# Kernel optimization log

Hardware: AMD Instinct MI355X
Metric: run time of the kernel (lower is better)

Reference implementation:

```python
import jax, jax.numpy as jnp
import numpy as np

B, C_IN, C_HID, H, W = 4, 512, 512, 64, 64


def setup_inputs() -> dict:
    key = jax.random.key(0)
    ks = jax.random.split(key, 9)
    s_in = 1.0 / np.sqrt(C_IN)
    s_hid = 1.0 / np.sqrt(C_HID)
    return {
        "inp": jax.random.normal(ks[0], (B, C_IN, H, W), dtype=jnp.float32),
        "Wk": jax.random.normal(ks[1], (C_HID, C_IN), dtype=jnp.float32) * s_in,
        "bk": jax.random.normal(ks[2], (C_HID,), dtype=jnp.float32) * 0.01,
        "Wq": jax.random.normal(ks[3], (C_HID, C_IN), dtype=jnp.float32) * s_in,
        "bq": jax.random.normal(ks[4], (C_HID,), dtype=jnp.float32) * 0.01,
        "Wv": jax.random.normal(ks[5], (C_HID, C_IN), dtype=jnp.float32) * s_in,
        "bv": jax.random.normal(ks[6], (C_HID,), dtype=jnp.float32) * 0.01,
        "Wo": jax.random.normal(ks[7], (C_IN, C_HID), dtype=jnp.float32) * s_hid,
        "bo": jax.random.normal(ks[8], (C_IN,), dtype=jnp.float32) * 0.01,
    }


def reference(inp, Wk, bk, Wq, bq, Wv, bv, Wo, bo):
    b, _, h, w = inp.shape
    n = h * w

    def conv1x1(x, Wt, bias):  # 1x1 conv == per-pixel GEMM
        return jnp.einsum('bchw,oc->bohw', x, Wt) + bias[None, :, None, None]

    k = conv1x1(inp, Wk, bk).reshape(b, C_HID, n)   # [B,Ch,N]
    q = conv1x1(inp, Wq, bq).reshape(b, C_HID, n)
    v = conv1x1(inp, Wv, bv).reshape(b, C_HID, n)

    scale = 1.0 / jnp.sqrt(jnp.asarray(C_HID, dtype=jnp.float32))
    # weight[b,i,j] = <key_i, query_j> / sqrt(Ch); softmax over j (dim=2)
    scores = jnp.einsum('bci,bcj->bij', k, q) * scale  # [B,N,N]
    weight = jax.nn.softmax(scores, axis=2)
    # out[b,c,i] = sum_j weight[b,i,j] * v[b,c,j]
    out = jnp.einsum('bij,bcj->bci', weight, v).reshape(b, C_HID, h, w)
    return conv1x1(out, Wo, bo)  # [B,C_in,H,W]
```

## Files before the change

### kernel.cpp

```cpp
#include <hip/hip_runtime.h>
#include <hip/hip_bf16.h>


typedef __attribute__((ext_vector_type(4))) float f32x4;
typedef __attribute__((ext_vector_type(8))) short short8;
typedef __attribute__((ext_vector_type(4))) short short4v;

#define QSCALE 0.06376639774f
#define FENCE asm volatile("" ::: "memory")
#define SBAR  __builtin_amdgcn_s_barrier()

__device__ __forceinline__ unsigned short f2bf(float f) {
  unsigned u = __builtin_bit_cast(unsigned, f);
  unsigned r = (u + 0x7FFFu + ((u >> 16) & 1u)) >> 16;
  return (unsigned short)r;
}

__device__ __forceinline__ void gll16(const void* g, void* l) {
  __builtin_amdgcn_global_load_lds((const __attribute__((address_space(1))) void*)g,
                                   (__attribute__((address_space(3))) void*)l, 16, 0, 0);
}

#define MFMA_BF16(d, va, vb) \
  d = __builtin_amdgcn_mfma_f32_16x16x32_bf16(va, vb, d, 0, 0, 0)

__device__ __forceinline__ void gemm256_core(
    const short* __restrict__ A, int lda,
    const short* __restrict__ B, int ldb,
    int nkt, char* sm, f32x4 (&acc)[8][4]) {
  const int tid = threadIdx.x, w = tid >> 6, lane = tid & 63;
  const int g = lane >> 4, l15 = lane & 15;
  const int wm = w >> 2, wn = w & 3;
  const int swz = (l15 & 7) << 4;
  const int brow = (wn & 1) << 6;

  auto stageA = [&](int buf, int h, int kt) {
    char* dst = sm + (((buf << 1) | h) << 14) + (w << 10);
    const char* gs = (const char*)A + ((size_t)(h * 128) * lda + (size_t)kt * 64) * 2;
#pragma unroll
    for (int q = 0; q < 2; ++q) {
      int o = (q << 13) | (w << 10) | (lane << 4);
      int row = o >> 7, cb = (o & 127) ^ ((row & 7) << 4);
      gll16(gs + (size_t)row * (lda * 2) + cb, dst + (q << 13));
    }
  };
  auto stageB = [&](int buf, int h, int kt) {
    char* dst = sm + 65536 + (((buf << 1) | h) << 14) + (w << 10);
    const char* gs = (const char*)B + ((size_t)(h * 128) * ldb + (size_t)kt * 64) * 2;
#pragma unroll
    for (int q = 0; q < 2; ++q) {
      int o = (q << 13) | (w << 10) | (lane << 4);
      int row = o >> 7, cb = (o & 127) ^ ((row & 7) << 4);
      gll16(gs + (size_t)row * (ldb * 2) + cb, dst + (q << 13));
    }
  };

  stageA(0, 0, 0); stageA(0, 1, 0); stageB(0, 0, 0); stageB(0, 1, 0);
  stageA(1, 0, 1); stageA(1, 1, 1); stageB(1, 0, 1); stageB(1, 1, 1);
  asm volatile("s_waitcnt vmcnt(8)" ::: "memory");
  SBAR; FENCE;

  for (int t = 0; t < nkt; ++t) {
    const int buf = t & 1;
    const char* SA = sm + (((buf << 1) | wm) << 14);
    const char* SB = sm + 65536 + (((buf << 1) | (wn >> 1)) << 14);
    short8 a[8][2], b[4][2];
#pragma unroll
    for (int mf = 0; mf < 8; ++mf)
      a[mf][0] = *(const short8*)(SA + (mf * 16 + l15) * 128 + ((g * 16) ^ swz));
#pragma unroll
    for (int nf = 0; nf < 4; ++nf)
      b[nf][0] = *(const short8*)(SB + (brow + nf * 16 + l15) * 128 + ((g * 16) ^ swz));
#pragma unroll
    for (int mf = 0; mf < 8; ++mf)
      a[mf][1] = *(const short8*)(SA + (mf * 16 + l15) * 128 + ((64 + g * 16) ^ swz));
#pragma unroll
    for (int nf = 0; nf < 4; ++nf)
      b[nf][1] = *(const short8*)(SB + (brow + nf * 16 + l15) * 128 + ((64 + g * 16) ^ swz));
    __builtin_amdgcn_s_setprio(1);
#pragma unroll
    for (int mf = 0; mf < 4; ++mf)
#pragma unroll
      for (int nf = 0; nf < 4; ++nf)
        MFMA_BF16(acc[mf][nf], a[mf][0], b[nf][0]);
    __builtin_amdgcn_s_setprio(0);
    asm volatile("s_waitcnt lgkmcnt(0)" ::: "memory");
    SBAR; FENCE;
    if (t + 2 < nkt) { stageA(buf, 0, t + 2); stageA(buf, 1, t + 2); }
    __builtin_amdgcn_s_setprio(1);
#pragma unroll
    for (int mf = 4; mf < 8; ++mf)
#pragma unroll
      for (int nf = 0; nf < 4; ++nf)
        MFMA_BF16(acc[mf][nf], a[mf][0], b[nf][0]);
    __builtin_amdgcn_s_setprio(0);
    if (t + 2 < nkt) { stageB(buf, 0, t + 2); stageB(buf, 1, t + 2); }
    __builtin_amdgcn_s_setprio(1);
#pragma unroll
    for (int mf = 0; mf < 4; ++mf)
#pragma unroll
      for (int nf = 0; nf < 4; ++nf)
        MFMA_BF16(acc[mf][nf], a[mf][1], b[nf][1]);
#pragma unroll
    for (int mf = 4; mf < 8; ++mf)
#pragma unroll
      for (int nf = 0; nf < 4; ++nf)
        MFMA_BF16(acc[mf][nf], a[mf][1], b[nf][1]);
    __builtin_amdgcn_s_setprio(0);
    if (t + 2 < nkt)      asm volatile("s_waitcnt vmcnt(8)" ::: "memory");
    else if (t + 1 < nkt) asm volatile("s_waitcnt vmcnt(0)" ::: "memory");
    SBAR; FENCE;
  }
}

#define BOUNCE256_WRITE(smp, row, colb, val) \
  *(short*)((smp) + (row) * 512 + (((colb)) ^ (((row) & 7) << 4))) = (val)

__device__ __forceinline__ void bounce256_flush(const char* smp, short* gbase,
                                                int pitch ) {
  const int tid = threadIdx.x;
  SBAR; FENCE;
#pragma unroll
  for (int it = 0; it < 16; ++it) {
    int row = (tid >> 5) + it * 16;
    short8 v = *(const short8*)(smp + row * 512 + (((tid & 31) * 16) ^ ((row & 7) << 4)));
    *(short8*)(gbase + (size_t)row * pitch + (tid & 31) * 8) = v;
  }
}

__device__ __forceinline__ void gemm_core(const short* __restrict__ A, int lda,
                                          const short* __restrict__ B, int ldb,
                                          int nk, short* lds, f32x4 (&acc)[4][4]) {
  const int tid = threadIdx.x, w = tid >> 6, lane = tid & 63;
  const int g = lane >> 4, l15 = lane & 15;
  const int wr = w >> 1, wc = w & 1;
  const int rsub = lane >> 2, slot = lane & 3;
  char* la = (char*)lds;
  char* lb = (char*)(lds + 128 * 32);
  for (int ki = 0; ki < nk; ++ki) {
    const int k0 = ki * 32;
    __syncthreads();
#pragma unroll
    for (int q = 0; q < 2; ++q) {
      int qq = w * 2 + q;
      int row = qq * 16 + rsub;
      int soff = ((slot ^ (row & 3)) * 16);
      gll16((const char*)(A + (size_t)row * lda + k0) + soff, la + qq * 1024);
      gll16((const char*)(B + (size_t)row * ldb + k0) + soff, lb + qq * 1024);
    }
    __syncthreads();
    short8 am[4], bn[4];
#pragma unroll
    for (int m = 0; m < 4; ++m) {
      int row = wr * 64 + m * 16 + l15;
      am[m] = *(const short8*)(la + row * 64 + ((g * 16) ^ ((l15 & 3) << 4)));
    }
#pragma unroll
    for (int n = 0; n < 4; ++n) {
      int row = wc * 64 + n * 16 + l15;
      bn[n] = *(const short8*)(lb + row * 64 + ((g * 16) ^ ((l15 & 3) << 4)));
    }
#pragma unroll
    for (int m = 0; m < 4; ++m)
#pragma unroll
      for (int n = 0; n < 4; ++n)
        MFMA_BF16(acc[m][n], am[m], bn[n]);
  }
}

__global__ __launch_bounds__(256) void cvt_w_kernel(
    const float* __restrict__ wk, const float* __restrict__ wq,
    const float* __restrict__ wv, const float* __restrict__ wo,
    short* __restrict__ o) {
  int z = blockIdx.y;
  const float* s = (z == 0) ? wk : (z == 1) ? wq : (z == 2) ? wv : wo;
  int i = blockIdx.x * 256 + threadIdx.x;
  float4 f = ((const float4*)s)[i];
  short4v v;
  v[0] = (short)f2bf(f.x); v[1] = (short)f2bf(f.y);
  v[2] = (short)f2bf(f.z); v[3] = (short)f2bf(f.w);
  if (z < 3) {
    *(short4v*)(o + z * 262144 + i * 4) = v;
  } else {
    int idx = i * 4, co = idx >> 9, cc = idx & 511;
    short* base = o + 786432 + co * 1024 + cc;
    *(short4v*)base = v;
    *(short4v*)(base + 512) = v;
  }
}

__global__ __launch_bounds__(256) void transpose_x_kernel(
    const float* __restrict__ inp, short* __restrict__ xt) {
  __shared__ float t[32][33];
  int tx = threadIdx.x, ty = threadIdx.y;
  int n0 = blockIdx.x * 32, c0 = blockIdx.y * 32, b = blockIdx.z;
  const float* src = inp + ((size_t)(b * 512 + c0)) * 4096 + n0;
#pragma unroll
  for (int r = 0; r < 4; ++r) t[ty + r * 8][tx] = src[(ty + r * 8) * 4096 + tx];
  __syncthreads();
  short* dst = xt + ((size_t)((b << 12) + n0)) * 512 + c0;
#pragma unroll
  for (int r = 0; r < 4; ++r) dst[(ty + r * 8) * 512 + tx] = (short)f2bf(t[tx][ty + r * 8]);
}

__global__ __launch_bounds__(512, 2) void kqv256_kernel(
    const short* __restrict__ xt,
    const short* __restrict__ wk, const short* __restrict__ wq, const short* __restrict__ wv,
    const float* __restrict__ bk, const float* __restrict__ bq, const float* __restrict__ bv,
    short* __restrict__ kt, short* __restrict__ qt, short* __restrict__ vc) {
  extern __shared__ char sm[];
  const int bid = blockIdx.x;
  const int xcd = bid & 7, s = bid >> 3;
  const int pg = s / 6, t = s % 6;
  const int panel = pg * 8 + xcd;
  const int z = (t < 4) ? (t >> 1) : 2;
  const short *A, *B;
  int arow0, brow0;
  if (z < 2) {
    arow0 = panel * 256; brow0 = (t & 1) * 256;
    A = xt + (size_t)arow0 * 512;
    B = ((z == 0) ? wk : wq) + (size_t)brow0 * 512;
  } else {
    arow0 = (t - 4) * 256; brow0 = panel * 256;
    A = wv + (size_t)arow0 * 512;
    B = xt + (size_t)brow0 * 512;
  }
  f32x4 acc[8][4] = {};
  gemm256_core(A, 512, B, 512, 8, sm, acc);
  const int tid = threadIdx.x, w = tid >> 6, lane = tid & 63;
  const int gq = lane >> 4, l15 = lane & 15;
  const int wm = w >> 2, wn = w & 3;
#pragma unroll
  for (int mf = 0; mf < 8; ++mf)
#pragma unroll
    for (int nf = 0; nf < 4; ++nf)
#pragma unroll
      for (int r = 0; r < 4; ++r) {
        int row = wm * 128 + mf * 16 + gq * 4 + r;
        int col = wn * 64 + nf * 16 + l15;
        float v = acc[mf][nf][r], val;
        if (z == 0)      val = (v + bk[brow0 + col]) * QSCALE;
        else if (z == 1) val = v + bq[brow0 + col];
        else             val = v + bv[arow0 + row];
        BOUNCE256_WRITE(sm, row, col * 2, (short)f2bf(val));
      }
  short* gbase; int pitch;
  if (z == 0)      { gbase = kt + (size_t)arow0 * 512 + brow0; pitch = 512; }
  else if (z == 1) { gbase = qt + (size_t)arow0 * 512 + brow0; pitch = 512; }
  else             { gbase = vc + (size_t)arow0 * 16384 + brow0; pitch = 16384; }
  bounce256_flush(sm, gbase, pitch);
}

__global__ __launch_bounds__(512, 2) void gemm_s256_kernel(
    const short* __restrict__ kt, const short* __restrict__ qt,
    short* __restrict__ P, float* __restrict__ Lpart) {
  extern __shared__ char sm[];
  const int bid = blockIdx.x;
  const int xcd = bid & 7, s = bid >> 3;
  const int b = xcd >> 1, h = xcd & 1;
  const int jt0 = (s & 7) * 256, i0 = (s >> 3) * 256;
  const short* A = kt + ((size_t)(b << 12) + i0) * 512;
  const short* B = qt + ((size_t)((b << 12) + h * 2048 + jt0)) * 512;
  f32x4 acc[8][4] = {};
  gemm256_core(A, 512, B, 512, 8, sm, acc);
  const int tid = threadIdx.x, w = tid >> 6, lane = tid & 63;
  const int gq = lane >> 4, l15 = lane & 15;
  const int wm = w >> 2, wn = w & 3;
  const int jp = (h * 2048 + jt0 + wn * 64) >> 6;
  float* Lp = Lpart + (((size_t)b * 64 + jp) << 12) + i0 + wm * 128;
#pragma unroll
  for (int mf = 0; mf < 8; ++mf) {
    float psum[4] = {0.f, 0.f, 0.f, 0.f};
#pragma unroll
    for (int nf = 0; nf < 4; ++nf)
#pragma unroll
      for (int r = 0; r < 4; ++r) {
        float p = exp2f(acc[mf][nf][r]);
        psum[r] += p;
        int row = wm * 128 + mf * 16 + gq * 4 + r;
        int colb = (wn * 64 + nf * 16 + l15) * 2;
        BOUNCE256_WRITE(sm, row, colb, (short)f2bf(p));
      }
#pragma unroll
    for (int r = 0; r < 4; ++r) {
      float ss = psum[r];
      ss += __shfl_xor(ss, 1); ss += __shfl_xor(ss, 2);
      ss += __shfl_xor(ss, 4); ss += __shfl_xor(ss, 8);
      if (l15 == 0) Lp[mf * 16 + gq * 4 + r] = ss;
    }
  }
  short* gbase = P + (size_t)h * 33554432 + ((size_t)((b << 12) + i0)) * 2048 + jt0;
  bounce256_flush(sm, gbase, 2048);
}

__global__ __launch_bounds__(512, 2) void gemm_pv256_kernel(
    const short* __restrict__ P, const short* __restrict__ vc,
    short* __restrict__ otab) {
  extern __shared__ char sm[];
  const int bid = blockIdx.x;
  const int xcd = bid & 7, s = bid >> 3;
  const int b = xcd >> 1, h = xcd & 1;
  const int c0 = (s & 1) * 256, i0 = (s >> 1) * 256;
  const short* A = P + (size_t)h * 33554432 + ((size_t)((b << 12) + i0)) * 2048;
  const short* B = vc + (size_t)c0 * 16384 + (b << 12) + h * 2048;
  f32x4 acc[8][4] = {};
  gemm256_core(A, 2048, B, 16384, 32, sm, acc);
  const int tid = threadIdx.x, w = tid >> 6, lane = tid & 63;
  const int gq = lane >> 4, l15 = lane & 15;
  const int wm = w >> 2, wn = w & 3;
#pragma unroll
  for (int mf = 0; mf < 8; ++mf)
#pragma unroll
    for (int nf = 0; nf < 4; ++nf)
#pragma unroll
      for (int r = 0; r < 4; ++r) {
        int row = wm * 128 + mf * 16 + gq * 4 + r;
        int colb = (wn * 64 + nf * 16 + l15) * 2;
        BOUNCE256_WRITE(sm, row, colb, (short)f2bf(acc[mf][nf][r]));
      }
  short* gbase = otab + ((size_t)((b << 12) + i0)) * 1024 + h * 512 + c0;
  bounce256_flush(sm, gbase, 1024);
}

__global__ __launch_bounds__(256) void lred_kernel(
    const float* __restrict__ Lpart, float* __restrict__ linv) {
  int i = blockIdx.x * 256 + threadIdx.x;
  int b = i >> 12;
  float s = 0.f;
#pragma unroll 8
  for (int jp = 0; jp < 64; ++jp) s += Lpart[(((size_t)b * 64 + jp) << 12) + (i & 4095)];
  linv[i] = 1.0f / s;
}

__global__ __launch_bounds__(256) void gemm_out_kernel(
    const short* __restrict__ wdup, const short* __restrict__ otab,
    const float* __restrict__ bo, const float* __restrict__ linv,
    float* __restrict__ out) {
  __shared__ short lds[2 * 128 * 32];
  const int bid = blockIdx.x;
  const int xcd = bid & 7, s = bid >> 3;
  const int cot = s & 3;
  const int p = (s >> 2) * 8 + xcd;
  const int nt = p & 31, b = p >> 5;
  const int arow0 = cot * 128;
  const int bn0 = nt * 128;
  const short* A = wdup + (size_t)arow0 * 1024;
  const short* B = otab + ((size_t)((b << 12) + bn0)) * 1024;
  f32x4 acc[4][4] = {};
  gemm_core(A, 1024, B, 1024, 32, lds, acc);
  const int tid = threadIdx.x, w = tid >> 6, lane = tid & 63;
  const int g = lane >> 4, l15 = lane & 15;
  const int wr = w >> 1, wc = w & 1;
#pragma unroll
  for (int m = 0; m < 4; ++m) {
    int co = arow0 + wr * 64 + m * 16 + g * 4;
#pragma unroll
    for (int n = 0; n < 4; ++n) {
      int nl = bn0 + wc * 64 + n * 16 + l15;
      float li = linv[(b << 12) + nl];
#pragma unroll
      for (int r = 0; r < 4; ++r)
        out[((size_t)(b * 512 + co + r) << 12) + nl] = acc[m][n][r] * li + bo[co + r];
    }
  }
}

extern "C" void kernel_launch(void* const* d_in, const int* in_sizes, int n_in,
                              void* d_out, int out_size, void* d_ws, size_t ws_size,
                              hipStream_t stream) {
  const float* inp = (const float*)d_in[0];
  const float* Wk = (const float*)d_in[1];
  const float* bk = (const float*)d_in[2];
  const float* Wq = (const float*)d_in[3];
  const float* bq = (const float*)d_in[4];
  const float* Wv = (const float*)d_in[5];
  const float* bv = (const float*)d_in[6];
  const float* Wo = (const float*)d_in[7];
  const float* bo = (const float*)d_in[8];
  float* out = (float*)d_out;
  char* ws = (char*)d_ws;
  const size_t MB = 1048576;
  short* kt    = (short*)(ws);
  short* qt    = (short*)(ws + 16 * MB);
  short* vc    = (short*)(ws + 32 * MB);
  short* wb    = (short*)(ws + 48 * MB);
  short* xt    = (short*)(ws + 51 * MB);
  float* Lpart = (float*)(ws + 51 * MB);
  float* linv  = (float*)(ws + 55 * MB);
  short* P     = (short*)(ws + 67 * MB);
  short* otab  = (short*)(ws + 195 * MB);

  (void)in_sizes; (void)n_in; (void)out_size; (void)ws_size;

  hipFuncSetAttribute((const void*)kqv256_kernel,
                      hipFuncAttributeMaxDynamicSharedMemorySize, 131072);
  hipFuncSetAttribute((const void*)gemm_s256_kernel,
                      hipFuncAttributeMaxDynamicSharedMemorySize, 131072);
  hipFuncSetAttribute((const void*)gemm_pv256_kernel,
                      hipFuncAttributeMaxDynamicSharedMemorySize, 131072);

  cvt_w_kernel<<<dim3(256, 4), 256, 0, stream>>>(Wk, Wq, Wv, Wo, wb);
  transpose_x_kernel<<<dim3(128, 16, 4), dim3(32, 8, 1), 0, stream>>>(inp, xt);
  kqv256_kernel<<<384, 512, 131072, stream>>>(
      xt, wb, wb + 262144, wb + 524288, bk, bq, bv, kt, qt, vc);
  gemm_s256_kernel<<<1024, 512, 131072, stream>>>(kt, qt, P, Lpart);
  gemm_pv256_kernel<<<256, 512, 131072, stream>>>(P, vc, otab);
  lred_kernel<<<64, 256, 0, stream>>>(Lpart, linv);
  gemm_out_kernel<<<512, 256, 0, stream>>>(wb + 786432, otab, bo, linv, out);
}
```

Before: 273.4 us.

## Use fine-grained interleaved staging pipeline in 256 GEMM core and port output GEMM

```diff
diff --git a/kernel.cpp b/kernel.cpp
--- a/kernel.cpp
+++ b/kernel.cpp
@@ -8,7 +8,8 @@
 
 #define QSCALE 0.06376639774f
 #define FENCE asm volatile("" ::: "memory")
-#define SBAR  __builtin_amdgcn_s_barrier()
+#define SBAR  do { FENCE; __builtin_amdgcn_s_barrier(); FENCE; } while (0)
+#define LGKM0 asm volatile("s_waitcnt lgkmcnt(0)" ::: "memory")
 
 __device__ __forceinline__ unsigned short f2bf(float f) {
   unsigned u = __builtin_bit_cast(unsigned, f);
@@ -24,7 +25,7 @@
 #define MFMA_BF16(d, va, vb) \
   d = __builtin_amdgcn_mfma_f32_16x16x32_bf16(va, vb, d, 0, 0, 0)
 
-__device__ __forceinline__ void gemm256_core(
+__device__ __forceinline__ void gemm256_fine(
     const short* __restrict__ A, int lda,
     const short* __restrict__ B, int ldb,
     int nkt, char* sm, f32x4 (&acc)[8][4]) {
@@ -33,83 +34,68 @@
   const int wm = w >> 2, wn = w & 3;
   const int swz = (l15 & 7) << 4;
   const int brow = (wn & 1) << 6;
-
-  auto stageA = [&](int buf, int h, int kt) {
-    char* dst = sm + (((buf << 1) | h) << 14) + (w << 10);
-    const char* gs = (const char*)A + ((size_t)(h * 128) * lda + (size_t)kt * 64) * 2;
+  const char* SAb = sm + (wm << 14);
+  const char* SBb = sm + 65536 + ((wn >> 1) << 14);
+
+  auto stage = [&](int mat, int half, int t) {
+    if (t >= nkt) return;
+    char* dst = sm + mat * 65536 + ((t & 1) << 15) + (half << 14) + (w << 10);
+    const short* src = mat ? B : A;
+    const int ld = mat ? ldb : lda;
+    const char* gs = (const char*)src + ((size_t)(half * 128) * ld + (size_t)t * 64) * 2;
 #pragma unroll
     for (int q = 0; q < 2; ++q) {
       int o = (q << 13) | (w << 10) | (lane << 4);
       int row = o >> 7, cb = (o & 127) ^ ((row & 7) << 4);
-      gll16(gs + (size_t)row * (lda * 2) + cb, dst + (q << 13));
+      gll16(gs + (size_t)row * (ld * 2) + cb, dst + (q << 13));
     }
   };
-  auto stageB = [&](int buf, int h, int kt) {
-    char* dst = sm + 65536 + (((buf << 1) | h) << 14) + (w << 10);
-    const char* gs = (const char*)B + ((size_t)(h * 128) * ldb + (size_t)kt * 64) * 2;
-#pragma unroll
-    for (int q = 0; q < 2; ++q) {
-      int o = (q << 13) | (w << 10) | (lane << 4);
-      int row = o >> 7, cb = (o & 127) ^ ((row & 7) << 4);
-      gll16(gs + (size_t)row * (ldb * 2) + cb, dst + (q << 13));
-    }
+  auto rdA = [&](short8* a4, int mf0, int ks, int buf) {
+    const char* SA = SAb + (buf << 15);
+#pragma unroll
+    for (int i = 0; i < 4; ++i)
+      a4[i] = *(const short8*)(SA + ((mf0 + i) * 16 + l15) * 128 + ((ks * 64 + g * 16) ^ swz));
   };
-
-  stageA(0, 0, 0); stageA(0, 1, 0); stageB(0, 0, 0); stageB(0, 1, 0);
-  stageA(1, 0, 1); stageA(1, 1, 1); stageB(1, 0, 1); stageB(1, 1, 1);
-  asm volatile("s_waitcnt vmcnt(8)" ::: "memory");
-  SBAR; FENCE;
-
-  for (int t = 0; t < nkt; ++t) {
-    const int buf = t & 1;
-    const char* SA = sm + (((buf << 1) | wm) << 14);
-    const char* SB = sm + 65536 + (((buf << 1) | (wn >> 1)) << 14);
-    short8 a[8][2], b[4][2];
-#pragma unroll
-    for (int mf = 0; mf < 8; ++mf)
-      a[mf][0] = *(const short8*)(SA + (mf * 16 + l15) * 128 + ((g * 16) ^ swz));
+  auto rdB = [&](short8* b4, int ks, int buf) {
+    const char* SB = SBb + (buf << 15);
 #pragma unroll
     for (int nf = 0; nf < 4; ++nf)
-      b[nf][0] = *(const short8*)(SB + (brow + nf * 16 + l15) * 128 + ((g * 16) ^ swz));
-#pragma unroll
-    for (int mf = 0; mf < 8; ++mf)
-      a[mf][1] = *(const short8*)(SA + (mf * 16 + l15) * 128 + ((64 + g * 16) ^ swz));
-#pragma unroll
-    for (int nf = 0; nf < 4; ++nf)
-      b[nf][1] = *(const short8*)(SB + (brow + nf * 16 + l15) * 128 + ((64 + g * 16) ^ swz));
+      b4[nf] = *(const short8*)(SB + (brow + nf * 16 + l15) * 128 + ((ks * 64 + g * 16) ^ swz));
+  };
+  auto mm = [&](short8* a4, short8* b4, int mf0) {
     __builtin_amdgcn_s_setprio(1);
 #pragma unroll
-    for (int mf = 0; mf < 4; ++mf)
+    for (int i = 0; i < 4; ++i)
 #pragma unroll
       for (int nf = 0; nf < 4; ++nf)
-        MFMA_BF16(acc[mf][nf], a[mf][0], b[nf][0]);
+        MFMA_BF16(acc[mf0 + i][nf], a4[i], b4[nf]);
     __builtin_amdgcn_s_setprio(0);
-    asm volatile("s_waitcnt lgkmcnt(0)" ::: "memory");
-    SBAR; FENCE;
-    if (t + 2 < nkt) { stageA(buf, 0, t + 2); stageA(buf, 1, t + 2); }
-    __builtin_amdgcn_s_setprio(1);
-#pragma unroll
-    for (int mf = 4; mf < 8; ++mf)
-#pragma unroll
-      for (int nf = 0; nf < 4; ++nf)
-        MFMA_BF16(acc[mf][nf], a[mf][0], b[nf][0]);
-    __builtin_amdgcn_s_setprio(0);
-    if (t + 2 < nkt) { stageB(buf, 0, t + 2); stageB(buf, 1, t + 2); }
-    __builtin_amdgcn_s_setprio(1);
-#pragma unroll
-    for (int mf = 0; mf < 4; ++mf)
-#pragma unroll
-      for (int nf = 0; nf < 4; ++nf)
-        MFMA_BF16(acc[mf][nf], a[mf][1], b[nf][1]);
-#pragma unroll
-    for (int mf = 4; mf < 8; ++mf)
-#pragma unroll
-      for (int nf = 0; nf < 4; ++nf)
-        MFMA_BF16(acc[mf][nf], a[mf][1], b[nf][1]);
-    __builtin_amdgcn_s_setprio(0);
-    if (t + 2 < nkt)      asm volatile("s_waitcnt vmcnt(8)" ::: "memory");
-    else if (t + 1 < nkt) asm volatile("s_waitcnt vmcnt(0)" ::: "memory");
-    SBAR; FENCE;
+  };
+
+  stage(1, 0, 0); stage(1, 1, 0); stage(0, 0, 0); stage(0, 1, 0); stage(1, 0, 1);
+
+  for (int T = 0; T < nkt; T += 2) {
+    short8 a[8], bb[4];
+    asm volatile("s_waitcnt vmcnt(2)" ::: "memory"); SBAR;
+    rdA(a, 0, 0, 0); rdB(bb, 0, 0); stage(1, 1, T + 1);
+    SBAR; LGKM0; mm(a, bb, 0); SBAR;
+    rdA(a + 4, 4, 0, 0); stage(0, 0, T + 1);
+    SBAR; LGKM0; mm(a + 4, bb, 4); SBAR;
+    rdA(a, 0, 1, 0); rdB(bb, 1, 0); stage(0, 1, T + 1);
+    SBAR; LGKM0; mm(a, bb, 0); SBAR;
+    rdA(a + 4, 4, 1, 0); stage(1, 0, T + 2);
+    SBAR; LGKM0; mm(a + 4, bb, 4); SBAR;
+    if (T + 2 < nkt) { asm volatile("s_waitcnt vmcnt(2)" ::: "memory"); }
+    else             { asm volatile("s_waitcnt vmcnt(0)" ::: "memory"); }
+    SBAR;
+    rdA(a, 0, 0, 1); rdB(bb, 0, 1); stage(1, 1, T + 2);
+    SBAR; LGKM0; mm(a, bb, 0); SBAR;
+    rdA(a + 4, 4, 0, 1); stage(0, 0, T + 2);
+    SBAR; LGKM0; mm(a + 4, bb, 4); SBAR;
+    rdA(a, 0, 1, 1); rdB(bb, 1, 1); stage(0, 1, T + 2);
+    SBAR; LGKM0; mm(a, bb, 0); SBAR;
+    rdA(a + 4, 4, 1, 1); stage(1, 0, T + 3);
+    SBAR; LGKM0; mm(a + 4, bb, 4); SBAR;
   }
 }
 
@@ -119,52 +105,12 @@
 __device__ __forceinline__ void bounce256_flush(const char* smp, short* gbase,
                                                 int pitch ) {
   const int tid = threadIdx.x;
-  SBAR; FENCE;
+  SBAR;
 #pragma unroll
   for (int it = 0; it < 16; ++it) {
     int row = (tid >> 5) + it * 16;
     short8 v = *(const short8*)(smp + row * 512 + (((tid & 31) * 16) ^ ((row & 7) << 4)));
     *(short8*)(gbase + (size_t)row * pitch + (tid & 31) * 8) = v;
-  }
-}
-
-__device__ __forceinline__ void gemm_core(const short* __restrict__ A, int lda,
-                                          const short* __restrict__ B, int ldb,
-                                          int nk, short* lds, f32x4 (&acc)[4][4]) {
-  const int tid = threadIdx.x, w = tid >> 6, lane = tid & 63;
-  const int g = lane >> 4, l15 = lane & 15;
-  const int wr = w >> 1, wc = w & 1;
-  const int rsub = lane >> 2, slot = lane & 3;
-  char* la = (char*)lds;
-  char* lb = (char*)(lds + 128 * 32);
-  for (int ki = 0; ki < nk; ++ki) {
-    const int k0 = ki * 32;
-    __syncthreads();
-#pragma unroll
-    for (int q = 0; q < 2; ++q) {
-      int qq = w * 2 + q;
-      int row = qq * 16 + rsub;
-      int soff = ((slot ^ (row & 3)) * 16);
-      gll16((const char*)(A + (size_t)row * lda + k0) + soff, la + qq * 1024);
-      gll16((const char*)(B + (size_t)row * ldb + k0) + soff, lb + qq * 1024);
-    }
-    __syncthreads();
-    short8 am[4], bn[4];
-#pragma unroll
-    for (int m = 0; m < 4; ++m) {
-      int row = wr * 64 + m * 16 + l15;
-      am[m] = *(const short8*)(la + row * 64 + ((g * 16) ^ ((l15 & 3) << 4)));
-    }
-#pragma unroll
-    for (int n = 0; n < 4; ++n) {
-      int row = wc * 64 + n * 16 + l15;
-      bn[n] = *(const short8*)(lb + row * 64 + ((g * 16) ^ ((l15 & 3) << 4)));
-    }
-#pragma unroll
-    for (int m = 0; m < 4; ++m)
-#pragma unroll
-      for (int n = 0; n < 4; ++n)
-        MFMA_BF16(acc[m][n], am[m], bn[n]);
   }
 }
 
@@ -226,7 +172,7 @@
     B = xt + (size_t)brow0 * 512;
   }
   f32x4 acc[8][4] = {};
-  gemm256_core(A, 512, B, 512, 8, sm, acc);
+  gemm256_fine(A, 512, B, 512, 8, sm, acc);
   const int tid = threadIdx.x, w = tid >> 6, lane = tid & 63;
   const int gq = lane >> 4, l15 = lane & 15;
   const int wm = w >> 2, wn = w & 3;
@@ -262,7 +208,7 @@
   const short* A = kt + ((size_t)(b << 12) + i0) * 512;
   const short* B = qt + ((size_t)((b << 12) + h * 2048 + jt0)) * 512;
   f32x4 acc[8][4] = {};
-  gemm256_core(A, 512, B, 512, 8, sm, acc);
+  gemm256_fine(A, 512, B, 512, 8, sm, acc);
   const int tid = threadIdx.x, w = tid >> 6, lane = tid & 63;
   const int gq = lane >> 4, l15 = lane & 15;
   const int wm = w >> 2, wn = w & 3;
@@ -304,7 +250,7 @@
   const short* A = P + (size_t)h * 33554432 + ((size_t)((b << 12) + i0)) * 2048;
   const short* B = vc + (size_t)c0 * 16384 + (b << 12) + h * 2048;
   f32x4 acc[8][4] = {};
-  gemm256_core(A, 2048, B, 16384, 32, sm, acc);
+  gemm256_fine(A, 2048, B, 16384, 32, sm, acc);
   const int tid = threadIdx.x, w = tid >> 6, lane = tid & 63;
   const int gq = lane >> 4, l15 = lane & 15;
   const int wm = w >> 2, wn = w & 3;
@@ -332,35 +278,33 @@
   linv[i] = 1.0f / s;
 }
 
-__global__ __launch_bounds__(256) void gemm_out_kernel(
+__global__ __launch_bounds__(512, 2) void out256_kernel(
     const short* __restrict__ wdup, const short* __restrict__ otab,
     const float* __restrict__ bo, const float* __restrict__ linv,
     float* __restrict__ out) {
-  __shared__ short lds[2 * 128 * 32];
+  extern __shared__ char sm[];
   const int bid = blockIdx.x;
-  const int xcd = bid & 7, s = bid >> 3;
-  const int cot = s & 3;
-  const int p = (s >> 2) * 8 + xcd;
-  const int nt = p & 31, b = p >> 5;
-  const int arow0 = cot * 128;
-  const int bn0 = nt * 128;
+  const int xcd = bid & 7, nt = bid >> 3;
+  const int b = xcd >> 1, cot = xcd & 1;
+  const int arow0 = cot * 256;
+  const int bn0 = nt * 256;
   const short* A = wdup + (size_t)arow0 * 1024;
   const short* B = otab + ((size_t)((b << 12) + bn0)) * 1024;
-  f32x4 acc[4][4] = {};
-  gemm_core(A, 1024, B, 1024, 32, lds, acc);
-  const int tid = threadIdx.x, w = tid >> 6, lane = tid & 63;
-  const int g = lane >> 4, l15 = lane & 15;
-  const int wr = w >> 1, wc = w & 1;
-#pragma unroll
-  for (int m = 0; m < 4; ++m) {
-    int co = arow0 + wr * 64 + m * 16 + g * 4;
-#pragma unroll
-    for (int n = 0; n < 4; ++n) {
-      int nl = bn0 + wc * 64 + n * 16 + l15;
+  f32x4 acc[8][4] = {};
+  gemm256_fine(A, 1024, B, 1024, 16, sm, acc);
+  const int tid = threadIdx.x, w = tid >> 6, lane = tid & 63;
+  const int gq = lane >> 4, l15 = lane & 15;
+  const int wm = w >> 2, wn = w & 3;
+#pragma unroll
+  for (int mf = 0; mf < 8; ++mf) {
+    int co = arow0 + wm * 128 + mf * 16 + gq * 4;
+#pragma unroll
+    for (int nf = 0; nf < 4; ++nf) {
+      int nl = bn0 + wn * 64 + nf * 16 + l15;
       float li = linv[(b << 12) + nl];
 #pragma unroll
       for (int r = 0; r < 4; ++r)
-        out[((size_t)(b * 512 + co + r) << 12) + nl] = acc[m][n][r] * li + bo[co + r];
+        out[((size_t)(b * 512 + co + r) << 12) + nl] = acc[mf][nf][r] * li + bo[co + r];
     }
   }
 }
@@ -398,6 +342,8 @@
                       hipFuncAttributeMaxDynamicSharedMemorySize, 131072);
   hipFuncSetAttribute((const void*)gemm_pv256_kernel,
                       hipFuncAttributeMaxDynamicSharedMemorySize, 131072);
+  hipFuncSetAttribute((const void*)out256_kernel,
+                      hipFuncAttributeMaxDynamicSharedMemorySize, 131072);
 
   cvt_w_kernel<<<dim3(256, 4), 256, 0, stream>>>(Wk, Wq, Wv, Wo, wb);
   transpose_x_kernel<<<dim3(128, 16, 4), dim3(32, 8, 1), 0, stream>>>(inp, xt);
@@ -406,5 +352,5 @@
   gemm_s256_kernel<<<1024, 512, 131072, stream>>>(kt, qt, P, Lpart);
   gemm_pv256_kernel<<<256, 512, 131072, stream>>>(P, vc, otab);
   lred_kernel<<<64, 256, 0, stream>>>(Lpart, linv);
-  gemm_out_kernel<<<512, 256, 0, stream>>>(wb + 786432, otab, bo, linv, out);
-}
+  out256_kernel<<<128, 512, 131072, stream>>>(wb + 786432, otab, bo, linv, out);
+}
```

Result: slower. 279.7 us (+2.3%).
